# Kernel optimization log

Hardware: AMD Instinct MI355X
Metric: run time of the kernel (lower is better)

## Reference

```python
import jax, jax.numpy as jnp
import numpy as np

B, N, FA, FP, C = 64, 64, 75, 14, 128


def _mlp2(x, W0, b0, W1, b1):
    # two lazy-Linear + ReLU sub-layers (n_sub_layer=2)
    h = jax.nn.relu(x @ W0 + b0)
    return jax.nn.relu(h @ W1 + b1)


def setup_inputs() -> dict:
    key = jax.random.key(0)
    ks = jax.random.split(key, 32)
    w = lambda k, s: jax.random.normal(k, s, jnp.float32) * 0.05
    inp = {
        "atom_x": jax.random.normal(ks[0], (B, N, FA), jnp.float32),
        "pair_x": jax.random.normal(ks[1], (B, N * N, FP), jnp.float32),
        # atom_to_atom: FA -> C -> C
        "a2a_W0": w(ks[2], (FA, C)), "a2a_b0": w(ks[3], (C,)),
        "a2a_W1": w(ks[4], (C, C)), "a2a_b1": w(ks[5], (C,)),
        # pair_to_atom: FP -> C -> C
        "p2a_W0": w(ks[6], (FP, C)), "p2a_b0": w(ks[7], (C,)),
        "p2a_W1": w(ks[8], (C, C)), "p2a_b1": w(ks[9], (C,)),
        # atom_layer: 2C -> C -> C
        "al_W0": w(ks[10], (2 * C, C)), "al_b0": w(ks[11], (C,)),
        "al_W1": w(ks[12], (C, C)), "al_b1": w(ks[13], (C,)),
        # atom_to_pair (weights shared across both orderings): 2FA -> C -> C
        "a2p_W0": w(ks[14], (2 * FA, C)), "a2p_b0": w(ks[15], (C,)),
        "a2p_W1": w(ks[16], (C, C)), "a2p_b1": w(ks[17], (C,)),
        # pair_to_pair: FP -> C -> C
        "p2p_W0": w(ks[18], (FP, C)), "p2p_b0": w(ks[19], (C,)),
        "p2p_W1": w(ks[20], (C, C)), "p2p_b1": w(ks[21], (C,)),
        # pair_layer: 2C -> C -> C
        "pl_W0": w(ks[22], (2 * C, C)), "pl_b0": w(ks[23], (C,)),
        "pl_W1": w(ks[24], (C, C)), "pl_b1": w(ks[25], (C,)),
    }
    return inp


def reference(atom_x, pair_x,
              a2a_W0, a2a_b0, a2a_W1, a2a_b1,
              p2a_W0, p2a_b0, p2a_W1, p2a_b1,
              al_W0, al_b0, al_W1, al_b1,
              a2p_W0, a2p_b0, a2p_W1, a2p_b1,
              p2p_W0, p2p_b0, p2p_W1, p2p_b1,
              pl_W0, pl_b0, pl_W1, pl_b1):
    b, n, fa = atom_x.shape
    # --- atom branch ---
    a0 = _mlp2(atom_x, a2a_W0, a2a_b0, a2a_W1, a2a_b1)            # [B,N,C]
    a1 = _mlp2(pair_x, p2a_W0, p2a_b0, p2a_W1, p2a_b1)            # [B,N*N,C]
    a1 = a1.reshape(b, n, n, -1).sum(axis=2)                      # PairToAtom sum
    a = jnp.concatenate([a0, a1], axis=-1)                        # [B,N,2C]
    next_atom = jax.nn.relu(_mlp2(a, al_W0, al_b0, al_W1, al_b1))  # extra relu per forward
    # --- pair branch ---
    rep = jnp.broadcast_to(atom_x[:, None, :, :], (b, n, n, fa))  # atom_repeat
    til = jnp.broadcast_to(atom_x[:, :, None, :], (b, n, n, fa))  # atom_tile
    pr0 = jnp.concatenate([til, rep], axis=-1).reshape(b, n * n, 2 * fa)
    pr1 = jnp.concatenate([rep, til], axis=-1).reshape(b, n * n, 2 * fa)
    p0 = (_mlp2(pr0, a2p_W0, a2p_b0, a2p_W1, a2p_b1)
          + _mlp2(pr1, a2p_W0, a2p_b0, a2p_W1, a2p_b1))            # [B,N*N,C]
    p1 = _mlp2(pair_x, p2p_W0, p2p_b0, p2p_W1, p2p_b1)            # [B,N*N,C]
    p = jnp.concatenate([p0, p1], axis=-1)                        # [B,N*N,2C]
    next_pair = jax.nn.relu(_mlp2(p, pl_W0, pl_b0, pl_W1, pl_b1))
    return (next_atom, next_pair)
```

## Files before the change

kernel.cpp:

```cpp
#include <hip/hip_runtime.h>
#include <hip/hip_bf16.h>

typedef unsigned short u16;
typedef unsigned int u32;
typedef __attribute__((ext_vector_type(8))) __bf16 bf16x8;
typedef __attribute__((ext_vector_type(4))) float f32x4;

#define B_ 64
#define N_ 64
#define FA_ 75
#define FP_ 14
#define C_ 128

__device__ float g_A0[4096 * 128];
__device__ float g_A1[4096 * 128];
__device__ float g_TB[4096 * 256];
__device__ u16   g_Wf[208896];
__device__ int   g_isbf;

#define OFF_AA0   0
#define OFF_AA1   12288
#define OFF_APT   28672
#define OFF_APB   40960
#define OFF_PA0   53248
#define OFF_PA1   57344
#define OFF_AL0   73728
#define OFF_AL1   106496
#define OFF_AP1   122880
#define OFF_PP0   139264
#define OFF_PP1   143360
#define OFF_PL0T  159744
#define OFF_PL0B  176128
#define OFF_PL1   192512

__device__ __forceinline__ float bf2f(u16 a) {
    union { u32 u; float f; } v; v.u = ((u32)a) << 16; return v.f;
}
__device__ __forceinline__ u16 f2bf(float f) {
    union { float f; u32 u; } v; v.f = f;
    u32 r = v.u + 0x7fffu + ((v.u >> 16) & 1u);
    return (u16)(r >> 16);
}
#if __has_builtin(__builtin_amdgcn_cvt_pk_bf16_f32)
__device__ __forceinline__ u32 f2bf_pk(float a, float b) {
    auto r = __builtin_amdgcn_cvt_pk_bf16_f32(a, b);
    if constexpr (sizeof(r) == 4) {
        union { decltype(r) v; u32 u; } c; c.v = r; return c.u;
    } else {
        return (u32)f2bf(a) | ((u32)f2bf(b) << 16);
    }
}
#else
__device__ __forceinline__ u32 f2bf_pk(float a, float b) {
    return (u32)f2bf(a) | ((u32)f2bf(b) << 16);
}
#endif

__device__ __forceinline__ u16 ldw(const void* p, size_t i, bool isbf) {
    if (isbf) return ((const u16*)p)[i];
    return f2bf(((const float*)p)[i]);
}
__device__ __forceinline__ float ldf(const void* p, size_t i, bool isbf) {
    if (isbf) return bf2f(((const u16*)p)[i]);
    return ((const float*)p)[i];
}
__device__ __forceinline__ f32x4 ldf4(const void* p, int i, bool isbf) {
    f32x4 r;
    if (isbf) {
        const u16* q = (const u16*)p + i;
        r[0] = bf2f(q[0]); r[1] = bf2f(q[1]); r[2] = bf2f(q[2]); r[3] = bf2f(q[3]);
    } else {
        r = *(const f32x4*)((const float*)p + i);
    }
    return r;
}
__device__ __forceinline__ uint4 pack8(const void* p, size_t base, int kmax, int k0, bool isbf) {
    uint4 u;
    if (isbf) {
        const u16* q = (const u16*)p + base;
        u16 h[8];
#pragma unroll
        for (int j = 0; j < 8; ++j) h[j] = (k0 + j < kmax) ? q[k0 + j] : (u16)0;
        u.x = (u32)h[0] | ((u32)h[1] << 16); u.y = (u32)h[2] | ((u32)h[3] << 16);
        u.z = (u32)h[4] | ((u32)h[5] << 16); u.w = (u32)h[6] | ((u32)h[7] << 16);
    } else {
        const float* q = (const float*)p + base;
        float f[8];
#pragma unroll
        for (int j = 0; j < 8; ++j) f[j] = (k0 + j < kmax) ? q[k0 + j] : 0.f;
        u.x = f2bf_pk(f[0], f[1]); u.y = f2bf_pk(f[2], f[3]);
        u.z = f2bf_pk(f[4], f[5]); u.w = f2bf_pk(f[6], f[7]);
    }
    return u;
}

__global__ void detect_k(const void* __restrict__ atom) {
    if (threadIdx.x == 0) {
        const u32* a = (const u32*)atom;
        int sane = 0;
        for (int w = 0; w < 64; ++w) {
            u32 ex = (a[w] >> 7) & 0xffu;
            sane += (ex >= 113u && ex <= 133u) ? 1 : 0;
        }
        g_isbf = (sane >= 32) ? 1 : 0;
    }
}

__global__ __launch_bounds__(256) void prep_w(
    const void* aaW0, const void* aaW1, const void* apW0,
    const void* paW0, const void* paW1, const void* alW0, const void* alW1,
    const void* apW1, const void* ppW0, const void* ppW1,
    const void* plW0, const void* plW1) {
    const void* srcs[14] = {aaW0, aaW1, apW0, apW0, paW0, paW1, alW0, alW1,
                            apW1, ppW0, ppW1, plW0, plW0, plW1};
    const int Ktab[14]  = {75, 128, 75, 75, 14, 128, 256, 128, 128, 14, 128, 128, 128, 128};
    const int KStab[14] = {3, 4, 3, 3, 1, 4, 8, 4, 4, 1, 4, 4, 4, 4};
    const int rofft[14] = {0, 0, 0, 75, 0, 0, 0, 0, 0, 0, 0, 0, 128, 0};
    const int baset[14] = {OFF_AA0, OFF_AA1, OFF_APT, OFF_APB, OFF_PA0, OFF_PA1,
                           OFF_AL0, OFF_AL1, OFF_AP1, OFF_PP0, OFF_PP1,
                           OFF_PL0T, OFF_PL0B, OFF_PL1};
    int gid = blockIdx.x * 256 + threadIdx.x;
    int j = 0, s = gid;
    while (j < 14 && s >= KStab[j] * 512) { s -= KStab[j] * 512; ++j; }
    if (j >= 14) return;
    const bool isbf = g_isbf != 0;
    int lane = s & 63, rest = s >> 6;
    int ks = rest % KStab[j], mt = rest / KStab[j];
    int m = mt * 16 + (lane & 15), q = lane >> 4;
    float f[8];
#pragma unroll
    for (int jj = 0; jj < 8; ++jj) {
        int k = ks * 32 + q * 8 + jj;
        f[jj] = (k < Ktab[j]) ? ldf(srcs[j], (size_t)(rofft[j] + k) * 128 + m, isbf) : 0.f;
    }
    uint4 u;
    u.x = f2bf_pk(f[0], f[1]); u.y = f2bf_pk(f[2], f[3]);
    u.z = f2bf_pk(f[4], f[5]); u.w = f2bf_pk(f[6], f[7]);
    *(uint4*)&g_Wf[(size_t)baset[j] + (size_t)s * 8] = u;
}

template<int KS, int NT>
__device__ __forceinline__ void gemm2(const u16* __restrict__ wf,
                                      const u16* __restrict__ bF,
                                      int mt0, int lane, f32x4 (&acc)[2][NT]) {
#pragma unroll
    for (int ks = 0; ks < KS; ++ks) {
        bf16x8 a0 = *(const bf16x8*)(wf + (((mt0    ) * KS + ks) * 64 + lane) * 8);
        bf16x8 a1 = *(const bf16x8*)(wf + (((mt0 + 1) * KS + ks) * 64 + lane) * 8);
#pragma unroll
        for (int nt = 0; nt < NT; ++nt) {
            bf16x8 b = *(const bf16x8*)(bF + ((nt * KS + ks) * 64 + lane) * 8);
            acc[0][nt] = __builtin_amdgcn_mfma_f32_16x16x32_bf16(a0, b, acc[0][nt], 0, 0, 0);
            acc[1][nt] = __builtin_amdgcn_mfma_f32_16x16x32_bf16(a1, b, acc[1][nt], 0, 0, 0);
        }
    }
}

__device__ __forceinline__ void frag_store(u16* dstF, int KSd, int nt, int mt, int lane, f32x4 v) {
    int c = lane & 15, quad = lane >> 4;
    int lp = c + 16 * ((2 * mt + (quad >> 1)) & 3);
    int ks = mt >> 1;
    uint2 u; u.x = f2bf_pk(v[0], v[1]); u.y = f2bf_pk(v[2], v[3]);
    *(uint2*)(dstF + (((nt * KSd + ks) * 64 + lp) * 8 + (quad & 1) * 4)) = u;
}

__device__ __forceinline__ void store_out4(void* outp, size_t elem, f32x4 v, bool isbf) {
    if (isbf) {
        uint2 u; u.x = f2bf_pk(v[0], v[1]); u.y = f2bf_pk(v[2], v[3]);
        *(uint2*)((u16*)outp + elem) = u;
    } else {
        *(f32x4*)((float*)outp + elem) = v;
    }
}

#define EPI_RELU_STORE(ACC, BB0, BB1, DST, NTN) do {                             \
    _Pragma("unroll") for (int ii = 0; ii < 2; ++ii) {                           \
        f32x4 bb_ = ii ? (BB1) : (BB0);                                          \
        _Pragma("unroll") for (int nt_ = 0; nt_ < NTN; ++nt_) {                  \
            f32x4 v_;                                                            \
            _Pragma("unroll") for (int r_ = 0; r_ < 4; ++r_) {                   \
                float x_ = ACC[ii][nt_][r_] + bb_[r_];                           \
                v_[r_] = x_ > 0.f ? x_ : 0.f;                                    \
            }                                                                    \
            frag_store(DST, 4, nt_, mt0 + ii, lane, v_);                         \
        }                                                                        \
    }                                                                            \
} while (0)

__global__ __launch_bounds__(256) void atom_pre(
    const void* __restrict__ atom,
    const void* __restrict__ aaB0, const void* __restrict__ aaB1) {
    __shared__ __align__(16) u16 sXF[4 * 3 * 64 * 8];
    __shared__ __align__(16) u16 sHF[4 * 4 * 64 * 8];
    const bool isbf = g_isbf != 0;
    const int t = threadIdx.x, lane = t & 63, w = t >> 6;
    const int quad = lane >> 4;
    const int b = blockIdx.x;
    for (int s = t; s < 4 * 3 * 64; s += 256) {
        int lane_s = s & 63, rest = s >> 6;
        int ks = rest % 3, nt = rest / 3;
        int n = nt * 16 + (lane_s & 15), q = lane_s >> 4;
        *(uint4*)&sXF[s * 8] = pack8(atom, (size_t)(b * 64 + n) * FA_, FA_, ks * 32 + q * 8, isbf);
    }
    __syncthreads();
    const int mt0 = 2 * w;
    {
        f32x4 bb0 = ldf4(aaB0, mt0 * 16 + quad * 4, isbf);
        f32x4 bb1 = ldf4(aaB0, (mt0 + 1) * 16 + quad * 4, isbf);
        f32x4 acc[2][4];
#pragma unroll
        for (int ii = 0; ii < 2; ++ii)
#pragma unroll
            for (int nt = 0; nt < 4; ++nt) acc[ii][nt] = (f32x4){0.f, 0.f, 0.f, 0.f};
        gemm2<3, 4>(g_Wf + OFF_AA0, sXF, mt0, lane, acc);
        EPI_RELU_STORE(acc, bb0, bb1, sHF, 4);
    }
    __syncthreads();
    {
        f32x4 bb0 = ldf4(aaB1, mt0 * 16 + quad * 4, isbf);
        f32x4 bb1 = ldf4(aaB1, (mt0 + 1) * 16 + quad * 4, isbf);
        f32x4 acc[2][4];
#pragma unroll
        for (int ii = 0; ii < 2; ++ii)
#pragma unroll
            for (int nt = 0; nt < 4; ++nt) acc[ii][nt] = (f32x4){0.f, 0.f, 0.f, 0.f};
        gemm2<4, 4>(g_Wf + OFF_AA1, sHF, mt0, lane, acc);
        int c = lane & 15;
#pragma unroll
        for (int ii = 0; ii < 2; ++ii) {
            int mt = mt0 + ii;
            f32x4 bb = ii ? bb1 : bb0;
#pragma unroll
            for (int nt = 0; nt < 4; ++nt) {
                f32x4 v;
#pragma unroll
                for (int r = 0; r < 4; ++r) { float x = acc[ii][nt][r] + bb[r]; v[r] = x > 0.f ? x : 0.f; }
                *(f32x4*)&g_A0[(size_t)(b * 64 + nt * 16 + c) * 128 + mt * 16 + quad * 4] = v;
            }
        }
    }
    {
        f32x4 accT[2][4], accB[2][4];
#pragma unroll
        for (int ii = 0; ii < 2; ++ii)
#pragma unroll
            for (int nt = 0; nt < 4; ++nt) { accT[ii][nt] = (f32x4){0.f,0.f,0.f,0.f}; accB[ii][nt] = (f32x4){0.f,0.f,0.f,0.f}; }
        gemm2<3, 4>(g_Wf + OFF_APT, sXF, mt0, lane, accT);
        gemm2<3, 4>(g_Wf + OFF_APB, sXF, mt0, lane, accB);
        int c = lane & 15;
#pragma unroll
        for (int ii = 0; ii < 2; ++ii) {
            int mt = mt0 + ii;
#pragma unroll
            for (int nt = 0; nt < 4; ++nt) {
                size_t row = (size_t)(b * 64 + nt * 16 + c);
                *(f32x4*)&g_TB[row * 256 + mt * 16 + quad * 4] = accT[ii][nt];
                *(f32x4*)&g_TB[row * 256 + 128 + mt * 16 + quad * 4] = accB[ii][nt];
            }
        }
    }
}

__global__ __launch_bounds__(256) void p2a_sum(
    const void* __restrict__ pairx,
    const void* __restrict__ paB0, const void* __restrict__ paB1) {
    __shared__ __align__(16) u16 sPF[4 * 1 * 64 * 8];
    __shared__ __align__(16) u16 sHF[4 * 4 * 64 * 8];
    const bool isbf = g_isbf != 0;
    const int t = threadIdx.x, lane = t & 63, w = t >> 6;
    const int quad = lane >> 4;
    const int bx = blockIdx.x;
    const size_t rbase = (size_t)bx * 64;
    {
        int lane_s = t & 63, nt = t >> 6;
        int n = nt * 16 + (lane_s & 15), q = lane_s >> 4;
        *(uint4*)&sPF[t * 8] = pack8(pairx, (rbase + n) * FP_, FP_, q * 8, isbf);
    }
    __syncthreads();
    const int mt0 = 2 * w;
    {
        f32x4 bb0 = ldf4(paB0, mt0 * 16 + quad * 4, isbf);
        f32x4 bb1 = ldf4(paB0, (mt0 + 1) * 16 + quad * 4, isbf);
        f32x4 acc[2][4];
#pragma unroll
        for (int ii = 0; ii < 2; ++ii)
#pragma unroll
            for (int nt = 0; nt < 4; ++nt) acc[ii][nt] = (f32x4){0.f, 0.f, 0.f, 0.f};
        gemm2<1, 4>(g_Wf + OFF_PA0, sPF, mt0, lane, acc);
        EPI_RELU_STORE(acc, bb0, bb1, sHF, 4);
    }
    __syncthreads();
    {
        f32x4 bb0 = ldf4(paB1, mt0 * 16 + quad * 4, isbf);
        f32x4 bb1 = ldf4(paB1, (mt0 + 1) * 16 + quad * 4, isbf);
        f32x4 acc[2][4];
#pragma unroll
        for (int ii = 0; ii < 2; ++ii)
#pragma unroll
            for (int nt = 0; nt < 4; ++nt) acc[ii][nt] = (f32x4){0.f, 0.f, 0.f, 0.f};
        gemm2<4, 4>(g_Wf + OFF_PA1, sHF, mt0, lane, acc);
#pragma unroll
        for (int ii = 0; ii < 2; ++ii) {
            int mt = mt0 + ii;
            f32x4 bb = ii ? bb1 : bb0;
            f32x4 ssum = (f32x4){0.f, 0.f, 0.f, 0.f};
#pragma unroll
            for (int nt = 0; nt < 4; ++nt)
#pragma unroll
                for (int r = 0; r < 4; ++r) {
                    float x = acc[ii][nt][r] + bb[r];
                    ssum[r] += (x > 0.f ? x : 0.f);
                }
#pragma unroll
            for (int m = 1; m < 16; m <<= 1)
#pragma unroll
                for (int r = 0; r < 4; ++r) ssum[r] += __shfl_xor(ssum[r], m, 64);
            if ((lane & 15) == 0)
                *(f32x4*)&g_A1[(size_t)bx * 128 + mt * 16 + quad * 4] = ssum;
        }
    }
}

__global__ __launch_bounds__(256) void atom_layer(
    const void* __restrict__ alB0, const void* __restrict__ alB1,
    void* __restrict__ out) {
    __shared__ __align__(16) u16 sXF[2 * 8 * 64 * 8];
    __shared__ __align__(16) u16 sHF[2 * 4 * 64 * 8];
    const bool isbf = g_isbf != 0;
    const int t = threadIdx.x, lane = t & 63, w = t >> 6;
    const int quad = lane >> 4;
    const int r0g = blockIdx.x * 32;
    for (int s = t; s < 2 * 8 * 64; s += 256) {
        int lane_s = s & 63, rest = s >> 6;
        int ks = rest & 7, nt = rest >> 3;
        int n = nt * 16 + (lane_s & 15), q = lane_s >> 4;
        int k0 = ks * 32 + q * 8;
        const float* src = (k0 < 128) ? &g_A0[(size_t)(r0g + n) * 128 + k0]
                                      : &g_A1[(size_t)(r0g + n) * 128 + (k0 - 128)];
        f32x4 f0 = *(const f32x4*)src, f1 = *(const f32x4*)(src + 4);
        uint4 u;
        u.x = f2bf_pk(f0[0], f0[1]); u.y = f2bf_pk(f0[2], f0[3]);
        u.z = f2bf_pk(f1[0], f1[1]); u.w = f2bf_pk(f1[2], f1[3]);
        *(uint4*)&sXF[s * 8] = u;
    }
    __syncthreads();
    const int mt0 = 2 * w;
    {
        f32x4 bb0 = ldf4(alB0, mt0 * 16 + quad * 4, isbf);
        f32x4 bb1 = ldf4(alB0, (mt0 + 1) * 16 + quad * 4, isbf);
        f32x4 acc[2][2];
#pragma unroll
        for (int ii = 0; ii < 2; ++ii)
#pragma unroll
            for (int nt = 0; nt < 2; ++nt) acc[ii][nt] = (f32x4){0.f, 0.f, 0.f, 0.f};
        gemm2<8, 2>(g_Wf + OFF_AL0, sXF, mt0, lane, acc);
        EPI_RELU_STORE(acc, bb0, bb1, sHF, 2);
    }
    __syncthreads();
    {
        f32x4 bb0 = ldf4(alB1, mt0 * 16 + quad * 4, isbf);
        f32x4 bb1 = ldf4(alB1, (mt0 + 1) * 16 + quad * 4, isbf);
        f32x4 acc[2][2];
#pragma unroll
        for (int ii = 0; ii < 2; ++ii)
#pragma unroll
            for (int nt = 0; nt < 2; ++nt) acc[ii][nt] = (f32x4){0.f, 0.f, 0.f, 0.f};
        gemm2<4, 2>(g_Wf + OFF_AL1, sHF, mt0, lane, acc);
        int c = lane & 15;
#pragma unroll
        for (int ii = 0; ii < 2; ++ii) {
            int mt = mt0 + ii;
            f32x4 bb = ii ? bb1 : bb0;
#pragma unroll
            for (int nt = 0; nt < 2; ++nt) {
                f32x4 v;
#pragma unroll
                for (int r = 0; r < 4; ++r) { float x = acc[ii][nt][r] + bb[r]; v[r] = x > 0.f ? x : 0.f; }
                store_out4(out, (size_t)(r0g + nt * 16 + c) * 128 + mt * 16 + quad * 4, v, isbf);
            }
        }
    }
}

__global__ __launch_bounds__(256, 4) void pair_fused(
    const void* __restrict__ pairx,
    const void* __restrict__ apB0, const void* __restrict__ apB1,
    const void* __restrict__ ppB0, const void* __restrict__ ppB1,
    const void* __restrict__ plB0, const void* __restrict__ plB1,
    void* __restrict__ out) {
    __shared__ __align__(16) u16 sPool[3 * 4096];
    u16* sX1 = sPool;
    u16* sX2 = sPool + 4096;
    u16* sR  = sPool + 8192;
    u16* sPrF = sR;
    float* sTip = (float*)(sR + 1024);
    float* sBip = sTip + 128;
    const bool isbf = g_isbf != 0;
    const int t = threadIdx.x, lane = t & 63, w = t >> 6;
    const int quad = lane >> 4, c = lane & 15;
    const int bx = blockIdx.x;
    const int b = bx >> 7, i = (bx >> 1) & 63, half = bx & 1;
    const int jbase = half * 32, trow = b * 64;
    const size_t prow0 = (size_t)b * 4096 + i * 64 + jbase;
    const int mt0 = 2 * w;

    if (t < 128) {
        float b0 = ldf(apB0, t, isbf);
        sTip[t] = g_TB[(size_t)(trow + i) * 256 + t] + b0;
        sBip[t] = g_TB[(size_t)(trow + i) * 256 + 128 + t] + b0;
    } else {
        int s = t - 128;
        int lane_s = s & 63, nt = s >> 6;
        int n = nt * 16 + (lane_s & 15), q = lane_s >> 4;
        *(uint4*)&sPrF[s * 8] = pack8(pairx, (prow0 + n) * FP_, FP_, q * 8, isbf);
    }
    __syncthreads();
    for (int sid = t; sid < 1024; sid += 256) {
        int buf = sid >> 9, s = sid & 511;
        int lane_s = s & 63, rest = s >> 6;
        int ks = rest & 3, nt = rest >> 2;
        int n = nt * 16 + (lane_s & 15), q = lane_s >> 4;
        int k0 = ks * 32 + q * 8;
        const float* Bj = &g_TB[(size_t)(trow + jbase + n) * 256];
        float v[8];
        if (buf == 0) {
#pragma unroll
            for (int j = 0; j < 8; ++j) { float x = sTip[k0 + j] + Bj[128 + k0 + j]; v[j] = x > 0.f ? x : 0.f; }
        } else {
#pragma unroll
            for (int j = 0; j < 8; ++j) { float x = Bj[k0 + j] + sBip[k0 + j]; v[j] = x > 0.f ? x : 0.f; }
        }
        uint4 u;
        u.x = f2bf_pk(v[0], v[1]); u.y = f2bf_pk(v[2], v[3]);
        u.z = f2bf_pk(v[4], v[5]); u.w = f2bf_pk(v[6], v[7]);
        *(uint4*)&(buf == 0 ? sX1 : sX2)[s * 8] = u;
    }
    f32x4 aH[2][2];
#pragma unroll
    for (int ii = 0; ii < 2; ++ii)
#pragma unroll
        for (int nt = 0; nt < 2; ++nt) aH[ii][nt] = (f32x4){0.f, 0.f, 0.f, 0.f};
    gemm2<1, 2>(g_Wf + OFF_PP0, sPrF, mt0, lane, aH);
    __syncthreads();
    {
        f32x4 bb0 = ldf4(apB1, mt0 * 16 + quad * 4, isbf);
        f32x4 bb1 = ldf4(apB1, (mt0 + 1) * 16 + quad * 4, isbf);
        f32x4 aA[2][2], aB[2][2];
#pragma unroll
        for (int ii = 0; ii < 2; ++ii)
#pragma unroll
            for (int nt = 0; nt < 2; ++nt) { aA[ii][nt] = (f32x4){0.f,0.f,0.f,0.f}; aB[ii][nt] = (f32x4){0.f,0.f,0.f,0.f}; }
        gemm2<4, 2>(g_Wf + OFF_AP1, sX1, mt0, lane, aA);
        gemm2<4, 2>(g_Wf + OFF_AP1, sX2, mt0, lane, aB);
#pragma unroll
        for (int ii = 0; ii < 2; ++ii) {
            int mt = mt0 + ii;
            f32x4 bb = ii ? bb1 : bb0;
#pragma unroll
            for (int nt = 0; nt < 2; ++nt) {
                f32x4 v;
#pragma unroll
                for (int r = 0; r < 4; ++r) {
                    float x = aA[ii][nt][r] + bb[r];
                    float y = aB[ii][nt][r] + bb[r];
                    v[r] = (x > 0.f ? x : 0.f) + (y > 0.f ? y : 0.f);
                }
                frag_store(sR, 4, nt, mt, lane, v);
            }
        }
    }
    __syncthreads();
    f32x4 C3[2][2];
#pragma unroll
    for (int ii = 0; ii < 2; ++ii)
#pragma unroll
        for (int nt = 0; nt < 2; ++nt) C3[ii][nt] = (f32x4){0.f, 0.f, 0.f, 0.f};
    gemm2<4, 2>(g_Wf + OFF_PL0T, sR, mt0, lane, C3);
    {
        f32x4 bb0 = ldf4(ppB0, mt0 * 16 + quad * 4, isbf);
        f32x4 bb1 = ldf4(ppB0, (mt0 + 1) * 16 + quad * 4, isbf);
        EPI_RELU_STORE(aH, bb0, bb1, sX1, 2);
    }
    __syncthreads();
    {
        f32x4 bb0 = ldf4(ppB1, mt0 * 16 + quad * 4, isbf);
        f32x4 bb1 = ldf4(ppB1, (mt0 + 1) * 16 + quad * 4, isbf);
        f32x4 aP[2][2];
#pragma unroll
        for (int ii = 0; ii < 2; ++ii)
#pragma unroll
            for (int nt = 0; nt < 2; ++nt) aP[ii][nt] = (f32x4){0.f, 0.f, 0.f, 0.f};
        gemm2<4, 2>(g_Wf + OFF_PP1, sX1, mt0, lane, aP);
        EPI_RELU_STORE(aP, bb0, bb1, sX2, 2);
    }
    __syncthreads();
    gemm2<4, 2>(g_Wf + OFF_PL0B, sX2, mt0, lane, C3);
    {
        f32x4 bb0 = ldf4(plB0, mt0 * 16 + quad * 4, isbf);
        f32x4 bb1 = ldf4(plB0, (mt0 + 1) * 16 + quad * 4, isbf);
        EPI_RELU_STORE(C3, bb0, bb1, sX1, 2);
    }
    __syncthreads();
    {
        f32x4 bb0 = ldf4(plB1, mt0 * 16 + quad * 4, isbf);
        f32x4 bb1 = ldf4(plB1, (mt0 + 1) * 16 + quad * 4, isbf);
        f32x4 aO[2][2];
#pragma unroll
        for (int ii = 0; ii < 2; ++ii)
#pragma unroll
            for (int nt = 0; nt < 2; ++nt) aO[ii][nt] = (f32x4){0.f, 0.f, 0.f, 0.f};
        gemm2<4, 2>(g_Wf + OFF_PL1, sX1, mt0, lane, aO);
        const size_t NA = (size_t)B_ * N_ * C_;
#pragma unroll
        for (int ii = 0; ii < 2; ++ii) {
            int mt = mt0 + ii;
            f32x4 bb = ii ? bb1 : bb0;
#pragma unroll
            for (int nt = 0; nt < 2; ++nt) {
                f32x4 v;
#pragma unroll
                for (int r = 0; r < 4; ++r) { float x = aO[ii][nt][r] + bb[r]; v[r] = x > 0.f ? x : 0.f; }
                store_out4(out, NA + (prow0 + nt * 16 + c) * 128 + mt * 16 + quad * 4, v, isbf);
            }
        }
    }
}

extern "C" void kernel_launch(void* const* d_in, const int* in_sizes, int n_in,
                              void* d_out, int out_size, void* d_ws, size_t ws_size,
                              hipStream_t stream) {
    const void* atom  = d_in[0];
    const void* pairx = d_in[1];
    const void* aaW0 = d_in[2];  const void* aaB0 = d_in[3];
    const void* aaW1 = d_in[4];  const void* aaB1 = d_in[5];
    const void* paW0 = d_in[6];  const void* paB0 = d_in[7];
    const void* paW1 = d_in[8];  const void* paB1 = d_in[9];
    const void* alW0 = d_in[10]; const void* alB0 = d_in[11];
    const void* alW1 = d_in[12]; const void* alB1 = d_in[13];
    const void* apW0 = d_in[14]; const void* apB0 = d_in[15];
    const void* apW1 = d_in[16]; const void* apB1 = d_in[17];
    const void* ppW0 = d_in[18]; const void* ppB0 = d_in[19];
    const void* ppW1 = d_in[20]; const void* ppB1 = d_in[21];
    const void* plW0 = d_in[22]; const void* plB0 = d_in[23];
    const void* plW1 = d_in[24]; const void* plB1 = d_in[25];
    (void)d_ws; (void)ws_size; (void)in_sizes; (void)n_in; (void)out_size;

    detect_k<<<1, 64, 0, stream>>>(atom);
    prep_w<<<102, 256, 0, stream>>>(aaW0, aaW1, apW0, paW0, paW1, alW0, alW1,
                                    apW1, ppW0, ppW1, plW0, plW1);
    atom_pre<<<64, 256, 0, stream>>>(atom, aaB0, aaB1);
    p2a_sum<<<4096, 256, 0, stream>>>(pairx, paB0, paB1);
    atom_layer<<<128, 256, 0, stream>>>(alB0, alB1, d_out);
    pair_fused<<<8192, 256, 0, stream>>>(pairx, apB0, apB1, ppB0, ppB1,
                                         plB0, plB1, d_out);
}
```

Before: 325.6 us.

## Retile pair_fused to 64 rows per block and split small atom kernels finer

pair_fused now processes 64 pair rows per block instead of 32, halving the grid to 4096 blocks. Each block reuses the weight fragments over twice as many MFMA tiles. The T/B broadcast inputs are built in registers with vectorised loads rather than staged through shared scalars. atom_pre and atom_layer go the other way, taking smaller row tiles and doubling their grids for more parallelism. In exchange, pair_fused uses more LDS and registers, and launch_bounds drops from 4 to 3 blocks per SM, which may reduce occupancy.

```diff
diff --git a/kernel.cpp b/kernel.cpp
--- a/kernel.cpp
+++ b/kernel.cpp
@@ -190,70 +190,70 @@
 __global__ __launch_bounds__(256) void atom_pre(
     const void* __restrict__ atom,
     const void* __restrict__ aaB0, const void* __restrict__ aaB1) {
-    __shared__ __align__(16) u16 sXF[4 * 3 * 64 * 8];
-    __shared__ __align__(16) u16 sHF[4 * 4 * 64 * 8];
+    __shared__ __align__(16) u16 sXF[2 * 3 * 64 * 8];
+    __shared__ __align__(16) u16 sHF[2 * 4 * 64 * 8];
     const bool isbf = g_isbf != 0;
     const int t = threadIdx.x, lane = t & 63, w = t >> 6;
     const int quad = lane >> 4;
-    const int b = blockIdx.x;
-    for (int s = t; s < 4 * 3 * 64; s += 256) {
+    const int r0g = blockIdx.x * 32;
+    for (int s = t; s < 2 * 3 * 64; s += 256) {
         int lane_s = s & 63, rest = s >> 6;
         int ks = rest % 3, nt = rest / 3;
         int n = nt * 16 + (lane_s & 15), q = lane_s >> 4;
-        *(uint4*)&sXF[s * 8] = pack8(atom, (size_t)(b * 64 + n) * FA_, FA_, ks * 32 + q * 8, isbf);
+        *(uint4*)&sXF[s * 8] = pack8(atom, (size_t)(r0g + n) * FA_, FA_, ks * 32 + q * 8, isbf);
     }
     __syncthreads();
     const int mt0 = 2 * w;
     {
         f32x4 bb0 = ldf4(aaB0, mt0 * 16 + quad * 4, isbf);
         f32x4 bb1 = ldf4(aaB0, (mt0 + 1) * 16 + quad * 4, isbf);
-        f32x4 acc[2][4];
-#pragma unroll
-        for (int ii = 0; ii < 2; ++ii)
-#pragma unroll
-            for (int nt = 0; nt < 4; ++nt) acc[ii][nt] = (f32x4){0.f, 0.f, 0.f, 0.f};
-        gemm2<3, 4>(g_Wf + OFF_AA0, sXF, mt0, lane, acc);
-        EPI_RELU_STORE(acc, bb0, bb1, sHF, 4);
+        f32x4 acc[2][2];
+#pragma unroll
+        for (int ii = 0; ii < 2; ++ii)
+#pragma unroll
+            for (int nt = 0; nt < 2; ++nt) acc[ii][nt] = (f32x4){0.f, 0.f, 0.f, 0.f};
+        gemm2<3, 2>(g_Wf + OFF_AA0, sXF, mt0, lane, acc);
+        EPI_RELU_STORE(acc, bb0, bb1, sHF, 2);
     }
     __syncthreads();
     {
         f32x4 bb0 = ldf4(aaB1, mt0 * 16 + quad * 4, isbf);
         f32x4 bb1 = ldf4(aaB1, (mt0 + 1) * 16 + quad * 4, isbf);
-        f32x4 acc[2][4];
-#pragma unroll
-        for (int ii = 0; ii < 2; ++ii)
-#pragma unroll
-            for (int nt = 0; nt < 4; ++nt) acc[ii][nt] = (f32x4){0.f, 0.f, 0.f, 0.f};
-        gemm2<4, 4>(g_Wf + OFF_AA1, sHF, mt0, lane, acc);
+        f32x4 acc[2][2];
+#pragma unroll
+        for (int ii = 0; ii < 2; ++ii)
+#pragma unroll
+            for (int nt = 0; nt < 2; ++nt) acc[ii][nt] = (f32x4){0.f, 0.f, 0.f, 0.f};
+        gemm2<4, 2>(g_Wf + OFF_AA1, sHF, mt0, lane, acc);
         int c = lane & 15;
 #pragma unroll
         for (int ii = 0; ii < 2; ++ii) {
             int mt = mt0 + ii;
             f32x4 bb = ii ? bb1 : bb0;
 #pragma unroll
-            for (int nt = 0; nt < 4; ++nt) {
+            for (int nt = 0; nt < 2; ++nt) {
                 f32x4 v;
 #pragma unroll
                 for (int r = 0; r < 4; ++r) { float x = acc[ii][nt][r] + bb[r]; v[r] = x > 0.f ? x : 0.f; }
-                *(f32x4*)&g_A0[(size_t)(b * 64 + nt * 16 + c) * 128 + mt * 16 + quad * 4] = v;
+                *(f32x4*)&g_A0[(size_t)(r0g + nt * 16 + c) * 128 + mt * 16 + quad * 4] = v;
             }
         }
     }
     {
-        f32x4 accT[2][4], accB[2][4];
-#pragma unroll
-        for (int ii = 0; ii < 2; ++ii)
-#pragma unroll
-            for (int nt = 0; nt < 4; ++nt) { accT[ii][nt] = (f32x4){0.f,0.f,0.f,0.f}; accB[ii][nt] = (f32x4){0.f,0.f,0.f,0.f}; }
-        gemm2<3, 4>(g_Wf + OFF_APT, sXF, mt0, lane, accT);
-        gemm2<3, 4>(g_Wf + OFF_APB, sXF, mt0, lane, accB);
+        f32x4 accT[2][2], accB[2][2];
+#pragma unroll
+        for (int ii = 0; ii < 2; ++ii)
+#pragma unroll
+            for (int nt = 0; nt < 2; ++nt) { accT[ii][nt] = (f32x4){0.f,0.f,0.f,0.f}; accB[ii][nt] = (f32x4){0.f,0.f,0.f,0.f}; }
+        gemm2<3, 2>(g_Wf + OFF_APT, sXF, mt0, lane, accT);
+        gemm2<3, 2>(g_Wf + OFF_APB, sXF, mt0, lane, accB);
         int c = lane & 15;
 #pragma unroll
         for (int ii = 0; ii < 2; ++ii) {
             int mt = mt0 + ii;
 #pragma unroll
-            for (int nt = 0; nt < 4; ++nt) {
-                size_t row = (size_t)(b * 64 + nt * 16 + c);
+            for (int nt = 0; nt < 2; ++nt) {
+                size_t row = (size_t)(r0g + nt * 16 + c);
                 *(f32x4*)&g_TB[row * 256 + mt * 16 + quad * 4] = accT[ii][nt];
                 *(f32x4*)&g_TB[row * 256 + 128 + mt * 16 + quad * 4] = accB[ii][nt];
             }
@@ -324,16 +324,15 @@
 __global__ __launch_bounds__(256) void atom_layer(
     const void* __restrict__ alB0, const void* __restrict__ alB1,
     void* __restrict__ out) {
-    __shared__ __align__(16) u16 sXF[2 * 8 * 64 * 8];
-    __shared__ __align__(16) u16 sHF[2 * 4 * 64 * 8];
+    __shared__ __align__(16) u16 sXF[1 * 8 * 64 * 8];
+    __shared__ __align__(16) u16 sHF[1 * 4 * 64 * 8];
     const bool isbf = g_isbf != 0;
     const int t = threadIdx.x, lane = t & 63, w = t >> 6;
     const int quad = lane >> 4;
-    const int r0g = blockIdx.x * 32;
-    for (int s = t; s < 2 * 8 * 64; s += 256) {
-        int lane_s = s & 63, rest = s >> 6;
-        int ks = rest & 7, nt = rest >> 3;
-        int n = nt * 16 + (lane_s & 15), q = lane_s >> 4;
+    const int r0g = blockIdx.x * 16;
+    for (int s = t; s < 8 * 64; s += 256) {
+        int lane_s = s & 63, ks = s >> 6;
+        int n = lane_s & 15, q = lane_s >> 4;
         int k0 = ks * 32 + q * 8;
         const float* src = (k0 < 128) ? &g_A0[(size_t)(r0g + n) * 128 + k0]
                                       : &g_A1[(size_t)(r0g + n) * 128 + (k0 - 128)];
@@ -348,116 +347,118 @@
     {
         f32x4 bb0 = ldf4(alB0, mt0 * 16 + quad * 4, isbf);
         f32x4 bb1 = ldf4(alB0, (mt0 + 1) * 16 + quad * 4, isbf);
-        f32x4 acc[2][2];
-#pragma unroll
-        for (int ii = 0; ii < 2; ++ii)
-#pragma unroll
-            for (int nt = 0; nt < 2; ++nt) acc[ii][nt] = (f32x4){0.f, 0.f, 0.f, 0.f};
-        gemm2<8, 2>(g_Wf + OFF_AL0, sXF, mt0, lane, acc);
-        EPI_RELU_STORE(acc, bb0, bb1, sHF, 2);
+        f32x4 acc[2][1];
+#pragma unroll
+        for (int ii = 0; ii < 2; ++ii) acc[ii][0] = (f32x4){0.f, 0.f, 0.f, 0.f};
+        gemm2<8, 1>(g_Wf + OFF_AL0, sXF, mt0, lane, acc);
+        EPI_RELU_STORE(acc, bb0, bb1, sHF, 1);
     }
     __syncthreads();
     {
         f32x4 bb0 = ldf4(alB1, mt0 * 16 + quad * 4, isbf);
         f32x4 bb1 = ldf4(alB1, (mt0 + 1) * 16 + quad * 4, isbf);
-        f32x4 acc[2][2];
-#pragma unroll
-        for (int ii = 0; ii < 2; ++ii)
-#pragma unroll
-            for (int nt = 0; nt < 2; ++nt) acc[ii][nt] = (f32x4){0.f, 0.f, 0.f, 0.f};
-        gemm2<4, 2>(g_Wf + OFF_AL1, sHF, mt0, lane, acc);
+        f32x4 acc[2][1];
+#pragma unroll
+        for (int ii = 0; ii < 2; ++ii) acc[ii][0] = (f32x4){0.f, 0.f, 0.f, 0.f};
+        gemm2<4, 1>(g_Wf + OFF_AL1, sHF, mt0, lane, acc);
         int c = lane & 15;
 #pragma unroll
         for (int ii = 0; ii < 2; ++ii) {
             int mt = mt0 + ii;
             f32x4 bb = ii ? bb1 : bb0;
-#pragma unroll
-            for (int nt = 0; nt < 2; ++nt) {
-                f32x4 v;
-#pragma unroll
-                for (int r = 0; r < 4; ++r) { float x = acc[ii][nt][r] + bb[r]; v[r] = x > 0.f ? x : 0.f; }
-                store_out4(out, (size_t)(r0g + nt * 16 + c) * 128 + mt * 16 + quad * 4, v, isbf);
-            }
-        }
-    }
-}
-
-__global__ __launch_bounds__(256, 4) void pair_fused(
+            f32x4 v;
+#pragma unroll
+            for (int r = 0; r < 4; ++r) { float x = acc[ii][0][r] + bb[r]; v[r] = x > 0.f ? x : 0.f; }
+            store_out4(out, (size_t)(r0g + c) * 128 + mt * 16 + quad * 4, v, isbf);
+        }
+    }
+}
+
+__global__ __launch_bounds__(256, 3) void pair_fused(
     const void* __restrict__ pairx,
     const void* __restrict__ apB0, const void* __restrict__ apB1,
     const void* __restrict__ ppB0, const void* __restrict__ ppB1,
     const void* __restrict__ plB0, const void* __restrict__ plB1,
     void* __restrict__ out) {
-    __shared__ __align__(16) u16 sPool[3 * 4096];
-    u16* sX1 = sPool;
-    u16* sX2 = sPool + 4096;
-    u16* sR  = sPool + 8192;
-    u16* sPrF = sR;
-    float* sTip = (float*)(sR + 1024);
-    float* sBip = sTip + 128;
+    __shared__ __align__(16) u16 sX1[4 * 4 * 64 * 8];
+    __shared__ __align__(16) u16 sX2[4 * 4 * 64 * 8];
+    __shared__ __align__(16) u16 sR [4 * 4 * 64 * 8];
+    __shared__ __align__(16) u16 sPr[4 * 1 * 64 * 8];
     const bool isbf = g_isbf != 0;
     const int t = threadIdx.x, lane = t & 63, w = t >> 6;
     const int quad = lane >> 4, c = lane & 15;
     const int bx = blockIdx.x;
-    const int b = bx >> 7, i = (bx >> 1) & 63, half = bx & 1;
-    const int jbase = half * 32, trow = b * 64;
-    const size_t prow0 = (size_t)b * 4096 + i * 64 + jbase;
+    const int b = bx >> 6, i = bx & 63;
+    const int trow = b * 64;
+    const size_t prow0 = (size_t)b * 4096 + (size_t)i * 64;
     const int mt0 = 2 * w;
 
-    if (t < 128) {
-        float b0 = ldf(apB0, t, isbf);
-        sTip[t] = g_TB[(size_t)(trow + i) * 256 + t] + b0;
-        sBip[t] = g_TB[(size_t)(trow + i) * 256 + 128 + t] + b0;
-    } else {
-        int s = t - 128;
-        int lane_s = s & 63, nt = s >> 6;
+    {
+        int lane_s = t & 63, nt = t >> 6;
         int n = nt * 16 + (lane_s & 15), q = lane_s >> 4;
-        *(uint4*)&sPrF[s * 8] = pack8(pairx, (prow0 + n) * FP_, FP_, q * 8, isbf);
-    }
-    __syncthreads();
-    for (int sid = t; sid < 1024; sid += 256) {
-        int buf = sid >> 9, s = sid & 511;
-        int lane_s = s & 63, rest = s >> 6;
-        int ks = rest & 3, nt = rest >> 2;
-        int n = nt * 16 + (lane_s & 15), q = lane_s >> 4;
-        int k0 = ks * 32 + q * 8;
-        const float* Bj = &g_TB[(size_t)(trow + jbase + n) * 256];
-        float v[8];
-        if (buf == 0) {
-#pragma unroll
-            for (int j = 0; j < 8; ++j) { float x = sTip[k0 + j] + Bj[128 + k0 + j]; v[j] = x > 0.f ? x : 0.f; }
-        } else {
-#pragma unroll
-            for (int j = 0; j < 8; ++j) { float x = Bj[k0 + j] + sBip[k0 + j]; v[j] = x > 0.f ? x : 0.f; }
-        }
-        uint4 u;
-        u.x = f2bf_pk(v[0], v[1]); u.y = f2bf_pk(v[2], v[3]);
-        u.z = f2bf_pk(v[4], v[5]); u.w = f2bf_pk(v[6], v[7]);
-        *(uint4*)&(buf == 0 ? sX1 : sX2)[s * 8] = u;
-    }
-    f32x4 aH[2][2];
+        *(uint4*)&sPr[t * 8] = pack8(pairx, (prow0 + n) * FP_, FP_, q * 8, isbf);
+    }
+    {
+        const int ksg = t >> 6;
+        const int k0 = ksg * 32 + quad * 8;
+        const int rc = c;
+        const float* TBi = &g_TB[(size_t)(trow + i) * 256 + k0];
+        f32x4 t0 = *(const f32x4*)TBi,        t1 = *(const f32x4*)(TBi + 4);
+        f32x4 o0 = *(const f32x4*)(TBi + 128), o1 = *(const f32x4*)(TBi + 132);
+        f32x4 b0a = ldf4(apB0, k0, isbf), b0b = ldf4(apB0, k0 + 4, isbf);
+        float Tip[8], Bip[8];
+#pragma unroll
+        for (int r = 0; r < 4; ++r) {
+            Tip[r] = t0[r] + b0a[r]; Tip[4 + r] = t1[r] + b0b[r];
+            Bip[r] = o0[r] + b0a[r]; Bip[4 + r] = o1[r] + b0b[r];
+        }
+#pragma unroll
+        for (int nt = 0; nt < 4; ++nt) {
+            int n = nt * 16 + rc;
+            const float* Bj = &g_TB[(size_t)(trow + n) * 256 + k0];
+            f32x4 j0 = *(const f32x4*)Bj,        j1 = *(const f32x4*)(Bj + 4);
+            f32x4 j2 = *(const f32x4*)(Bj + 128), j3 = *(const f32x4*)(Bj + 132);
+            float v0[8], v1[8];
+#pragma unroll
+            for (int r = 0; r < 4; ++r) {
+                float x0 = Tip[r] + j2[r];      v0[r]     = x0 > 0.f ? x0 : 0.f;
+                float x1 = Tip[4 + r] + j3[r];  v0[4 + r] = x1 > 0.f ? x1 : 0.f;
+                float y0 = j0[r] + Bip[r];      v1[r]     = y0 > 0.f ? y0 : 0.f;
+                float y1 = j1[r] + Bip[4 + r];  v1[4 + r] = y1 > 0.f ? y1 : 0.f;
+            }
+            uint4 u0, u1;
+            u0.x = f2bf_pk(v0[0], v0[1]); u0.y = f2bf_pk(v0[2], v0[3]);
+            u0.z = f2bf_pk(v0[4], v0[5]); u0.w = f2bf_pk(v0[6], v0[7]);
+            u1.x = f2bf_pk(v1[0], v1[1]); u1.y = f2bf_pk(v1[2], v1[3]);
+            u1.z = f2bf_pk(v1[4], v1[5]); u1.w = f2bf_pk(v1[6], v1[7]);
+            int slot = ((nt * 4 + ksg) * 64 + lane) * 8;
+            *(uint4*)&sX1[slot] = u0;
+            *(uint4*)&sX2[slot] = u1;
+        }
+    }
+    __syncthreads();
+    f32x4 aH[2][4];
 #pragma unroll
     for (int ii = 0; ii < 2; ++ii)
 #pragma unroll
-        for (int nt = 0; nt < 2; ++nt) aH[ii][nt] = (f32x4){0.f, 0.f, 0.f, 0.f};
-    gemm2<1, 2>(g_Wf + OFF_PP0, sPrF, mt0, lane, aH);
-    __syncthreads();
+        for (int nt = 0; nt < 4; ++nt) aH[ii][nt] = (f32x4){0.f, 0.f, 0.f, 0.f};
+    gemm2<1, 4>(g_Wf + OFF_PP0, sPr, mt0, lane, aH);
     {
         f32x4 bb0 = ldf4(apB1, mt0 * 16 + quad * 4, isbf);
         f32x4 bb1 = ldf4(apB1, (mt0 + 1) * 16 + quad * 4, isbf);
-        f32x4 aA[2][2], aB[2][2];
-#pragma unroll
-        for (int ii = 0; ii < 2; ++ii)
-#pragma unroll
-            for (int nt = 0; nt < 2; ++nt) { aA[ii][nt] = (f32x4){0.f,0.f,0.f,0.f}; aB[ii][nt] = (f32x4){0.f,0.f,0.f,0.f}; }
-        gemm2<4, 2>(g_Wf + OFF_AP1, sX1, mt0, lane, aA);
-        gemm2<4, 2>(g_Wf + OFF_AP1, sX2, mt0, lane, aB);
+        f32x4 aA[2][4], aB[2][4];
+#pragma unroll
+        for (int ii = 0; ii < 2; ++ii)
+#pragma unroll
+            for (int nt = 0; nt < 4; ++nt) { aA[ii][nt] = (f32x4){0.f,0.f,0.f,0.f}; aB[ii][nt] = (f32x4){0.f,0.f,0.f,0.f}; }
+        gemm2<4, 4>(g_Wf + OFF_AP1, sX1, mt0, lane, aA);
+        gemm2<4, 4>(g_Wf + OFF_AP1, sX2, mt0, lane, aB);
 #pragma unroll
         for (int ii = 0; ii < 2; ++ii) {
             int mt = mt0 + ii;
             f32x4 bb = ii ? bb1 : bb0;
 #pragma unroll
-            for (int nt = 0; nt < 2; ++nt) {
+            for (int nt = 0; nt < 4; ++nt) {
                 f32x4 v;
 #pragma unroll
                 for (int r = 0; r < 4; ++r) {
@@ -470,53 +471,53 @@
         }
     }
     __syncthreads();
-    f32x4 C3[2][2];
+    f32x4 C3[2][4];
 #pragma unroll
     for (int ii = 0; ii < 2; ++ii)
 #pragma unroll
-        for (int nt = 0; nt < 2; ++nt) C3[ii][nt] = (f32x4){0.f, 0.f, 0.f, 0.f};
-    gemm2<4, 2>(g_Wf + OFF_PL0T, sR, mt0, lane, C3);
+        for (int nt = 0; nt < 4; ++nt) C3[ii][nt] = (f32x4){0.f, 0.f, 0.f, 0.f};
+    gemm2<4, 4>(g_Wf + OFF_PL0T, sR, mt0, lane, C3);
     {
         f32x4 bb0 = ldf4(ppB0, mt0 * 16 + quad * 4, isbf);
         f32x4 bb1 = ldf4(ppB0, (mt0 + 1) * 16 + quad * 4, isbf);
-        EPI_RELU_STORE(aH, bb0, bb1, sX1, 2);
+        EPI_RELU_STORE(aH, bb0, bb1, sX1, 4);
     }
     __syncthreads();
     {
         f32x4 bb0 = ldf4(ppB1, mt0 * 16 + quad * 4, isbf);
         f32x4 bb1 = ldf4(ppB1, (mt0 + 1) * 16 + quad * 4, isbf);
-        f32x4 aP[2][2];
-#pragma unroll
-        for (int ii = 0; ii < 2; ++ii)
-#pragma unroll
-            for (int nt = 0; nt < 2; ++nt) aP[ii][nt] = (f32x4){0.f, 0.f, 0.f, 0.f};
-        gemm2<4, 2>(g_Wf + OFF_PP1, sX1, mt0, lane, aP);
-        EPI_RELU_STORE(aP, bb0, bb1, sX2, 2);
-    }
-    __syncthreads();
-    gemm2<4, 2>(g_Wf + OFF_PL0B, sX2, mt0, lane, C3);
+        f32x4 aP[2][4];
+#pragma unroll
+        for (int ii = 0; ii < 2; ++ii)
+#pragma unroll
+            for (int nt = 0; nt < 4; ++nt) aP[ii][nt] = (f32x4){0.f, 0.f, 0.f, 0.f};
+        gemm2<4, 4>(g_Wf + OFF_PP1, sX1, mt0, lane, aP);
+        EPI_RELU_STORE(aP, bb0, bb1, sX2, 4);
+    }
+    __syncthreads();
+    gemm2<4, 4>(g_Wf + OFF_PL0B, sX2, mt0, lane, C3);
     {
         f32x4 bb0 = ldf4(plB0, mt0 * 16 + quad * 4, isbf);
         f32x4 bb1 = ldf4(plB0, (mt0 + 1) * 16 + quad * 4, isbf);
-        EPI_RELU_STORE(C3, bb0, bb1, sX1, 2);
+        EPI_RELU_STORE(C3, bb0, bb1, sX1, 4);
     }
     __syncthreads();
     {
         f32x4 bb0 = ldf4(plB1, mt0 * 16 + quad * 4, isbf);
         f32x4 bb1 = ldf4(plB1, (mt0 + 1) * 16 + quad * 4, isbf);
-        f32x4 aO[2][2];
-#pragma unroll
-        for (int ii = 0; ii < 2; ++ii)
-#pragma unroll
-            for (int nt = 0; nt < 2; ++nt) aO[ii][nt] = (f32x4){0.f, 0.f, 0.f, 0.f};
-        gemm2<4, 2>(g_Wf + OFF_PL1, sX1, mt0, lane, aO);
+        f32x4 aO[2][4];
+#pragma unroll
+        for (int ii = 0; ii < 2; ++ii)
+#pragma unroll
+            for (int nt = 0; nt < 4; ++nt) aO[ii][nt] = (f32x4){0.f, 0.f, 0.f, 0.f};
+        gemm2<4, 4>(g_Wf + OFF_PL1, sX1, mt0, lane, aO);
         const size_t NA = (size_t)B_ * N_ * C_;
 #pragma unroll
         for (int ii = 0; ii < 2; ++ii) {
             int mt = mt0 + ii;
             f32x4 bb = ii ? bb1 : bb0;
 #pragma unroll
-            for (int nt = 0; nt < 2; ++nt) {
+            for (int nt = 0; nt < 4; ++nt) {
                 f32x4 v;
 #pragma unroll
                 for (int r = 0; r < 4; ++r) { float x = aO[ii][nt][r] + bb[r]; v[r] = x > 0.f ? x : 0.f; }
@@ -548,9 +549,9 @@
     detect_k<<<1, 64, 0, stream>>>(atom);
     prep_w<<<102, 256, 0, stream>>>(aaW0, aaW1, apW0, paW0, paW1, alW0, alW1,
                                     apW1, ppW0, ppW1, plW0, plW1);
-    atom_pre<<<64, 256, 0, stream>>>(atom, aaB0, aaB1);
+    atom_pre<<<128, 256, 0, stream>>>(atom, aaB0, aaB1);
     p2a_sum<<<4096, 256, 0, stream>>>(pairx, paB0, paB1);
-    atom_layer<<<128, 256, 0, stream>>>(alB0, alB1, d_out);
-    pair_fused<<<8192, 256, 0, stream>>>(pairx, apB0, apB1, ppB0, ppB1,
+    atom_layer<<<256, 256, 0, stream>>>(alB0, alB1, d_out);
+    pair_fused<<<4096, 256, 0, stream>>>(pairx, apB0, apB1, ppB0, ppB1,
                                          plB0, plB1, d_out);
 }
```

Result: faster. 308.0 us (-5.4%).
